# Kernel tuning notes

Measured on AMD Instinct MI355X. Metric: run time of the kernel, lower is better.

## Reference

```python
import jax, jax.numpy as jnp
import numpy as np

N_E = 8192
E_DIM = 64
BETA = 0.25
DIVERSITY_GAMMA = 1.0
INV_TEMP = 100.0
EPS = 1e-05


def _entropy(p):
    # matches torch: (-p * log(clamp(p, min=eps))).sum(-1)
    return (-p * jnp.log(jnp.clip(p, EPS))).sum(axis=-1)


def setup_inputs() -> dict:
    key = jax.random.key(0)
    k1, k2 = jax.random.split(key)
    z = jax.random.normal(k1, (16, E_DIM, 32, 32), dtype=jnp.float32)
    # codebook, init like nn.Embedding then uniform_(-1/n_e, 1/n_e) scale doesn't matter for math;
    # use a small uniform init faithful to the module
    emb = jax.random.uniform(k2, (N_E, E_DIM), dtype=jnp.float32,
                             minval=-1.0 / N_E, maxval=1.0 / N_E)
    return {"z": z, "emb": emb}


def reference(z, emb):
    sg = jax.lax.stop_gradient
    # b c h w -> b h w c
    zp = jnp.transpose(z, (0, 2, 3, 1))            # [B,H,W,C]
    zf = zp.reshape(-1, E_DIM)                      # [N, C]
    # pairwise squared distances: ||z||^2 + ||e||^2 - 2 z e^T
    d = (jnp.sum(zf * zf, axis=1, keepdims=True)
         + jnp.sum(emb * emb, axis=1)
         - 2.0 * jnp.einsum('nd,kd->nk', zf, emb))  # [N, n_e]
    min_indices = jnp.argmin(d, axis=1)             # [N]
    z_q = emb[min_indices].reshape(zp.shape)        # gather, [B,H,W,C]
    # legacy commitment loss
    loss = (jnp.mean((sg(z_q) - zp) ** 2)
            + BETA * jnp.mean((z_q - sg(zp)) ** 2))
    # entropy aux loss (frac_per_sample_entropy == 1.0)
    prob = jax.nn.softmax(-d * INV_TEMP, axis=-1)   # [N, n_e]
    per_sample_entropy = _entropy(prob).mean()
    avg_prob = prob.mean(axis=0)                    # [n_e]
    codebook_entropy = _entropy(avg_prob)
    entropy_aux = per_sample_entropy - DIVERSITY_GAMMA * codebook_entropy
    # straight-through estimator
    z_q = zp + sg(z_q - zp)
    quantized = jnp.transpose(z_q, (0, 3, 1, 2))    # b h w c -> b c h w
    return quantized, loss, entropy_aux, min_indices
```

## Files before the change

kernel.cpp:

```cpp
#include <hip/hip_runtime.h>
#include <cfloat>


typedef __attribute__((ext_vector_type(8))) short short8v;
typedef __attribute__((ext_vector_type(4))) float f32x4;

#define C100L2E 144.26950408889634f
#define C200L2E 288.53900817779268f
#define LN2 0.6931471805599453

#define BLOB_TILE 33792
#define OFF_BLOB   0
#define OFF_INVZ   2162688
#define OFF_MINIDX 2228224
#define OFF_AVG    2293760
#define OFF_PSE    2326528
#define OFF_ZPART  2326544
#define OFF_S1PART (OFF_ZPART + 262144)
#define OFF_DMPART (OFF_S1PART + 262144)
#define OFF_IMPART (OFF_DMPART + 262144)
#define OFF_LOSSP  (OFF_IMPART + 262144)
#define OFF_ZZ     (OFF_LOSSP + 32768)

__device__ __forceinline__ unsigned short f2bf_rne(float f) {
    unsigned u = __float_as_uint(f);
    u = (u + 0x7fffu + ((u >> 16) & 1u)) >> 16;
    return (unsigned short)u;
}

__device__ __forceinline__ void gload_lds16(const void* g, void* l) {
    __builtin_amdgcn_global_load_lds(
        (const __attribute__((address_space(1))) unsigned int*)g,
        (__attribute__((address_space(3))) unsigned int*)l, 16, 0, 0);
}

__global__ __launch_bounds__(256) void k_prep(const float* __restrict__ emb,
                                              char* __restrict__ blob) {
    const int k = blockIdx.x * 256 + threadIdx.x;
    const float* row = emb + k * 64;
    float fv[64];
#pragma unroll
    for (int i = 0; i < 16; ++i) {
        float4 v = ((const float4*)row)[i];
        fv[4 * i] = v.x; fv[4 * i + 1] = v.y; fv[4 * i + 2] = v.z; fv[4 * i + 3] = v.w;
    }
    float r8[8];
#pragma unroll
    for (int j = 0; j < 8; ++j) r8[j] = __fmul_rn(fv[j], fv[j]);
#pragma unroll
    for (int i = 8; i < 64; i += 8)
#pragma unroll
        for (int j = 0; j < 8; ++j)
            r8[j] = __fadd_rn(r8[j], __fmul_rn(fv[i + j], fv[i + j]));
    float s01 = __fadd_rn(r8[0], r8[1]), s23 = __fadd_rn(r8[2], r8[3]);
    float s45 = __fadd_rn(r8[4], r8[5]), s67 = __fadd_rn(r8[6], r8[7]);
    float e2 = __fadd_rn(__fadd_rn(s01, s23), __fadd_rn(s45, s67));

    char* tb = blob + (size_t)(k >> 7) * BLOB_TILE;
    const int r = k & 127;
    ((float*)(tb + 32768))[r] = e2;
    const int sw = (r & 7) << 4;
#pragma unroll
    for (int dh = 0; dh < 2; ++dh)
#pragma unroll
        for (int cg = 0; cg < 4; ++cg) {
            short8v hv, lv;
#pragma unroll
            for (int e = 0; e < 8; ++e) {
                float f = fv[dh * 32 + cg * 8 + e];
                unsigned short hb = f2bf_rne(f);
                float hf = __uint_as_float((unsigned)hb << 16);
                hv[e] = (short)hb;
                lv[e] = (short)f2bf_rne(f - hf);
            }
            const int byt = (r * 128 + dh * 64 + cg * 16) ^ sw;
            *(short8v*)(tb + byt) = hv;
            *(short8v*)(tb + 16384 + byt) = lv;
        }
}

__global__ __launch_bounds__(256) void k_zprep(const float* __restrict__ z,
                                               char* __restrict__ zblob,
                                               float* __restrict__ zz) {
    const int r = blockIdx.x * 256 + threadIdx.x;
    const float* src = z + (r >> 10) * 65536 + (r & 1023);
    float fv[64];
#pragma unroll
    for (int c = 0; c < 64; ++c) fv[c] = src[c * 1024];

    float r8[8];
#pragma unroll
    for (int j = 0; j < 8; ++j) r8[j] = __fmul_rn(fv[j], fv[j]);
#pragma unroll
    for (int i = 8; i < 64; i += 8)
#pragma unroll
        for (int j = 0; j < 8; ++j)
            r8[j] = __fadd_rn(r8[j], __fmul_rn(fv[i + j], fv[i + j]));
    float s01 = __fadd_rn(r8[0], r8[1]), s23 = __fadd_rn(r8[2], r8[3]);
    float s45 = __fadd_rn(r8[4], r8[5]), s67 = __fadd_rn(r8[6], r8[7]);
    zz[r] = __fadd_rn(__fadd_rn(s01, s23), __fadd_rn(s45, s67));

    char* tb = zblob + (size_t)(r >> 6) * 16384;
    const int rowp = r & 63;
#pragma unroll
    for (int cg = 0; cg < 8; ++cg) {
        short8v hv, lv;
#pragma unroll
        for (int e = 0; e < 8; ++e) {
            float f = fv[cg * 8 + e];
            unsigned short hb = f2bf_rne(f);
            float hf = __uint_as_float((unsigned)hb << 16);
            hv[e] = (short)hb;
            lv[e] = (short)f2bf_rne(f - hf);
        }
        *(short8v*)(tb + rowp * 128 + cg * 16) = hv;
        *(short8v*)(tb + 8192 + rowp * 128 + cg * 16) = lv;
    }
}

#define STAGE_EMB(DSTBASE, TILE)                                                  \
    {                                                                             \
        const char* gsrc = blob + (size_t)(TILE) * BLOB_TILE;                     \
        char* ldst = (DSTBASE) + ((tid >> 6) << 10);                              \
        const char* g = gsrc + tid * 16;                                          \
        _Pragma("unroll")                                                         \
        for (int q = 0; q < 8; ++q)                                               \
            gload_lds16(g + q * 4096, ldst + q * 4096);                           \
        if (tid < 32) gload_lds16(gsrc + 32768 + tid * 16, (DSTBASE) + 32768);    \
    }

#define STAGE512(DSTBASE, TILE)                                                   \
    {                                                                             \
        const char* gsrc = blob + (size_t)(TILE) * BLOB_TILE;                     \
        char* ldst = (DSTBASE) + ((tid >> 6) << 12);                              \
        const char* g = gsrc + ((tid >> 6) << 12) + (tid & 63) * 16;              \
        _Pragma("unroll")                                                         \
        for (int q = 0; q < 4; ++q)                                               \
            gload_lds16(g + q * 1024, ldst + q * 1024);                           \
        if (tid < 32) gload_lds16(gsrc + 32768 + tid * 16, (DSTBASE) + 32768);    \
    }

__global__ __launch_bounds__(512) void k_pass1(
    const char* __restrict__ zblob, const char* __restrict__ blob,
    const float* __restrict__ zz,
    float* __restrict__ Zpart, float* __restrict__ S1part,
    float* __restrict__ dmpart, int* __restrict__ impart)
{
    __shared__ __align__(16) char smem[2 * BLOB_TILE];

    const int tid = threadIdx.x;
    const int panel = blockIdx.x >> 2;
    const int ks = blockIdx.x & 3;
    const int n0 = panel * 128;

    const int ln = tid & 63, wv = tid >> 6;
    const int lr = ln & 15, lg = ln >> 4;

    short8v Ah[2], Al[2];
    {
        const int p64 = (n0 >> 6) + (wv >> 2);
        const int rowp = (wv & 3) * 16 + lr;
        const char* tb = zblob + (size_t)p64 * 16384;
#pragma unroll
        for (int s = 0; s < 2; ++s) {
            const int byt = rowp * 128 + s * 64 + lg * 16;
            Ah[s] = *(const short8v*)(tb + byt);
            Al[s] = *(const short8v*)(tb + 8192 + byt);
        }
    }
    float zzr[4];
#pragma unroll
    for (int rg = 0; rg < 4; ++rg)
        zzr[rg] = zz[n0 + wv * 16 + lg * 4 + rg];

    STAGE512(smem, ks * 16);

    float Zp[4] = {0.f, 0.f, 0.f, 0.f}, S1p[4] = {0.f, 0.f, 0.f, 0.f};
    float dmin[4] = {FLT_MAX, FLT_MAX, FLT_MAX, FLT_MAX};
    int imin[4] = {0, 0, 0, 0};

    for (int it = 0; it < 16; ++it) {
        const int kbase = ks * 2048 + it * 128;
        __syncthreads();
        const char* bb = smem + (it & 1) * BLOB_TILE;
        if (it < 15) STAGE512(smem + ((it + 1) & 1) * BLOB_TILE, ks * 16 + it + 1);

        f32x4 acc[8];
#pragma unroll
        for (int f = 0; f < 8; ++f) { f32x4 zv = {0.f, 0.f, 0.f, 0.f}; acc[f] = zv; }

#pragma unroll
        for (int f = 0; f < 8; ++f) {
            const int rr = f * 16 + lr;
            const int sw2 = (rr & 7) << 4;
            short8v Bh[2], Bl[2];
#pragma unroll
            for (int s = 0; s < 2; ++s) {
                const int byt = (rr * 128 + s * 64 + lg * 16) ^ sw2;
                Bh[s] = *(const short8v*)(bb + byt);
                Bl[s] = *(const short8v*)(bb + 16384 + byt);
            }
#pragma unroll
            for (int s = 0; s < 2; ++s) {
                acc[f] = __builtin_amdgcn_mfma_f32_16x16x32_bf16(Ah[s], Bh[s], acc[f], 0, 0, 0);
                acc[f] = __builtin_amdgcn_mfma_f32_16x16x32_bf16(Ah[s], Bl[s], acc[f], 0, 0, 0);
                acc[f] = __builtin_amdgcn_mfma_f32_16x16x32_bf16(Al[s], Bh[s], acc[f], 0, 0, 0);
                acc[f] = __builtin_amdgcn_mfma_f32_16x16x32_bf16(Al[s], Bl[s], acc[f], 0, 0, 0);
            }
        }

#pragma unroll
        for (int f = 0; f < 8; ++f) {
            const float e2v = *(const float*)(bb + 32768 + (f * 16 + lr) * 4);
            const float c2 = e2v * C100L2E;
            const int kk = kbase + f * 16 + lr;
#pragma unroll
            for (int rg = 0; rg < 4; ++rg) {
                const float sdot = acc[f][rg];
                const float t = fmaf(sdot, C200L2E, -c2);
                const float ex = __builtin_amdgcn_exp2f(t);
                Zp[rg] += ex;
                S1p[rg] = fmaf(t, ex, S1p[rg]);
                const float pre = __fadd_rn(zzr[rg], e2v);
                const float dnp = fmaf(-2.f, sdot, pre);
                if (dnp < dmin[rg]) { dmin[rg] = dnp; imin[rg] = kk; }
            }
        }
    }

#pragma unroll
    for (int msk = 1; msk < 16; msk <<= 1) {
#pragma unroll
        for (int rg = 0; rg < 4; ++rg) {
            float d2 = __shfl_xor(dmin[rg], msk, 16);
            int i2 = __shfl_xor(imin[rg], msk, 16);
            float Z2 = __shfl_xor(Zp[rg], msk, 16);
            float s2 = __shfl_xor(S1p[rg], msk, 16);
            if (d2 < dmin[rg] || (d2 == dmin[rg] && i2 < imin[rg])) {
                dmin[rg] = d2; imin[rg] = i2;
            }
            Zp[rg] += Z2;
            S1p[rg] += s2;
        }
    }
    if (lr == 0) {
#pragma unroll
        for (int rg = 0; rg < 4; ++rg) {
            const int n = n0 + wv * 16 + lg * 4 + rg;
            Zpart[ks * 16384 + n] = Zp[rg];
            S1part[ks * 16384 + n] = S1p[rg];
            dmpart[ks * 16384 + n] = dmin[rg];
            impart[ks * 16384 + n] = imin[rg];
        }
    }
}

__global__ __launch_bounds__(256) void k_rowred(
    const float* __restrict__ Zpart, const float* __restrict__ S1part,
    const float* __restrict__ dmpart, const int* __restrict__ impart,
    float* __restrict__ invZ, int* __restrict__ minidx,
    float* __restrict__ out_idx, double* __restrict__ pse_sum)
{
    const int n = blockIdx.x * 256 + threadIdx.x;
    float Z = __fadd_rn(__fadd_rn(Zpart[n], Zpart[16384 + n]),
                        __fadd_rn(Zpart[32768 + n], Zpart[49152 + n]));
    float S1 = __fadd_rn(__fadd_rn(S1part[n], S1part[16384 + n]),
                         __fadd_rn(S1part[32768 + n], S1part[49152 + n]));
    float dm = dmpart[n];
    int im = impart[n];
#pragma unroll
    for (int ksp = 1; ksp < 4; ++ksp) {
        float d2 = dmpart[ksp * 16384 + n];
        int i2 = impart[ksp * 16384 + n];
        if (d2 < dm || (d2 == dm && i2 < im)) { dm = d2; im = i2; }
    }
    minidx[n] = im;
    out_idx[n] = (float)im;
    float iz = 1.0f / Z;
    invZ[n] = iz;
    double h = log((double)Z) - LN2 * (double)S1 * (double)iz;
#pragma unroll
    for (int m = 32; m > 0; m >>= 1) h += __shfl_xor(h, m, 64);
    if ((threadIdx.x & 63) == 0) atomicAdd(pse_sum, h);
}

__global__ __launch_bounds__(256) void k_pass2(
    const char* __restrict__ zblob, const char* __restrict__ blob,
    const float* __restrict__ invZ, float* __restrict__ avg_acc)
{
    __shared__ __align__(16) char smem[BLOB_TILE + 4096];
    float* izAll = (float*)(smem + BLOB_TILE);

    const int tid = threadIdx.x;
    const int kt = blockIdx.x & 63;
    const int ns = blockIdx.x >> 6;
    const int ln = tid & 63, wv = tid >> 6;
    const int lr = ln & 15, lg = ln >> 4;

    STAGE_EMB(smem, kt);
    gload_lds16((const char*)(invZ + ns * 1024) + tid * 16,
                (char*)izAll + (wv << 10));
    __syncthreads();

    float e2v[8];
#pragma unroll
    for (int f = 0; f < 8; ++f)
        e2v[f] = *(const float*)(smem + 32768 + (f * 16 + lr) * 4);

    float acck[8] = {0.f, 0.f, 0.f, 0.f, 0.f, 0.f, 0.f, 0.f};

    for (int it = 0; it < 8; ++it) {
        short8v Ah[2][2], Al[2][2];
        const int p64 = ns * 16 + it * 2 + (wv >> 1);
        const char* tb = zblob + (size_t)p64 * 16384;
#pragma unroll
        for (int m = 0; m < 2; ++m) {
            const int rowp = (wv & 1) * 32 + m * 16 + lr;
#pragma unroll
            for (int s = 0; s < 2; ++s) {
                const int byt = rowp * 128 + s * 64 + lg * 16;
                Ah[m][s] = *(const short8v*)(tb + byt);
                Al[m][s] = *(const short8v*)(tb + 8192 + byt);
            }
        }
        const int izb = it * 128 + wv * 32 + lg * 4;
        float4 iz0 = *(const float4*)&izAll[izb];
        float4 iz1 = *(const float4*)&izAll[izb + 16];
        float izr[2][4] = {{iz0.x, iz0.y, iz0.z, iz0.w},
                           {iz1.x, iz1.y, iz1.z, iz1.w}};

        f32x4 acc[2][8];
#pragma unroll
        for (int m = 0; m < 2; ++m)
#pragma unroll
            for (int f = 0; f < 8; ++f) {
                f32x4 zv = {0.f, 0.f, 0.f, 0.f};
                acc[m][f] = zv;
            }

#pragma unroll
        for (int f = 0; f < 8; ++f) {
            const int rr = f * 16 + lr;
            const int sw2 = (rr & 7) << 4;
            short8v Bh[2], Bl[2];
#pragma unroll
            for (int s = 0; s < 2; ++s) {
                const int byt = (rr * 128 + s * 64 + lg * 16) ^ sw2;
                Bh[s] = *(const short8v*)(smem + byt);
                Bl[s] = *(const short8v*)(smem + 16384 + byt);
            }
#pragma unroll
            for (int s = 0; s < 2; ++s)
#pragma unroll
                for (int m = 0; m < 2; ++m) {
                    acc[m][f] = __builtin_amdgcn_mfma_f32_16x16x32_bf16(Ah[m][s], Bh[s], acc[m][f], 0, 0, 0);
                    acc[m][f] = __builtin_amdgcn_mfma_f32_16x16x32_bf16(Ah[m][s], Bl[s], acc[m][f], 0, 0, 0);
                    acc[m][f] = __builtin_amdgcn_mfma_f32_16x16x32_bf16(Al[m][s], Bh[s], acc[m][f], 0, 0, 0);
                    acc[m][f] = __builtin_amdgcn_mfma_f32_16x16x32_bf16(Al[m][s], Bl[s], acc[m][f], 0, 0, 0);
                }
        }

#pragma unroll
        for (int f = 0; f < 8; ++f) {
            const float c2 = e2v[f] * C100L2E;
#pragma unroll
            for (int m = 0; m < 2; ++m)
#pragma unroll
                for (int rg = 0; rg < 4; ++rg) {
                    const float t = fmaf(acc[m][f][rg], C200L2E, -c2);
                    const float ex = __builtin_amdgcn_exp2f(t);
                    acck[f] = fmaf(ex, izr[m][rg], acck[f]);
                }
        }
    }

#pragma unroll
    for (int f = 0; f < 8; ++f) {
        float cs = acck[f];
        cs += __shfl_xor(cs, 16, 64);
        cs += __shfl_xor(cs, 32, 64);
        if (lg == 0) atomicAdd(&avg_acc[kt * 128 + f * 16 + lr], cs);
    }
}

__global__ __launch_bounds__(256) void k_quant(
    const float* __restrict__ z, const float* __restrict__ emb,
    const int* __restrict__ minidx, float* __restrict__ out,
    double* __restrict__ loss_part)
{
    __shared__ float lred[4];
    const int o = blockIdx.x * 256 + threadIdx.x;
    const int n = ((o >> 16) << 10) + (o & 1023);
    const int c = (o >> 10) & 63;
    const int idx = minidx[n];
    const float e = emb[idx * 64 + c];
    const float zv = z[o];
    out[o] = e;
    float d = e - zv;
    float sq = d * d;
#pragma unroll
    for (int m = 32; m > 0; m >>= 1) sq += __shfl_xor(sq, m, 64);
    if ((threadIdx.x & 63) == 0) lred[threadIdx.x >> 6] = sq;
    __syncthreads();
    if (threadIdx.x == 0)
        loss_part[blockIdx.x] = (double)lred[0] + (double)lred[1]
                              + (double)lred[2] + (double)lred[3];
}

__global__ __launch_bounds__(256) void k_final(
    const float* __restrict__ avg_acc, const double* __restrict__ pse_sum,
    const double* __restrict__ loss_part, float* __restrict__ out)
{
    __shared__ double red[256];
    const int tid = threadIdx.x;

    double lsum = 0.0;
    for (int k = tid; k < 4096; k += 256) lsum += loss_part[k];
    red[tid] = lsum;
    __syncthreads();
    for (int s = 128; s > 0; s >>= 1) {
        if (tid < s) red[tid] += red[tid + s];
        __syncthreads();
    }
    double ltot = red[0];
    __syncthreads();

    double local = 0.0;
    for (int k = tid; k < 8192; k += 256) {
        float p = avg_acc[k] * (1.0f / 16384.0f);
        float cl = fmaxf(p, 1e-5f);
        local += (double)(-p * logf(cl));
    }
    red[tid] = local;
    __syncthreads();
    for (int s = 128; s > 0; s >>= 1) {
        if (tid < s) red[tid] += red[tid + s];
        __syncthreads();
    }
    if (tid == 0) {
        double ce = red[0];
        double pse = pse_sum[0] / 16384.0;
        out[1048576] = (float)(1.25 * ltot / 1048576.0);
        out[1048577] = (float)(pse - ce);
    }
}

extern "C" void kernel_launch(void* const* d_in, const int* in_sizes, int n_in,
                              void* d_out, int out_size, void* d_ws, size_t ws_size,
                              hipStream_t stream) {
    const float* z = (const float*)d_in[0];
    const float* emb = (const float*)d_in[1];
    float* out = (float*)d_out;
    char* ws = (char*)d_ws;
    char* blob = ws + OFF_BLOB;
    float* invZ = (float*)(ws + OFF_INVZ);
    int* minidx = (int*)(ws + OFF_MINIDX);
    float* avg_acc = (float*)(ws + OFF_AVG);
    double* pse_sum = (double*)(ws + OFF_PSE);
    float* Zpart = (float*)(ws + OFF_ZPART);
    float* S1part = (float*)(ws + OFF_S1PART);
    float* dmpart = (float*)(ws + OFF_DMPART);
    int* impart = (int*)(ws + OFF_IMPART);
    double* loss_part = (double*)(ws + OFF_LOSSP);
    float* zz = (float*)(ws + OFF_ZZ);
    char* zblob = (char*)d_out;

    hipMemsetAsync(ws + OFF_AVG, 0, 32768 + 16, stream);

    k_prep<<<32, 256, 0, stream>>>(emb, blob);
    k_zprep<<<64, 256, 0, stream>>>(z, zblob, zz);
    k_pass1<<<512, 512, 0, stream>>>(zblob, blob, zz, Zpart, S1part, dmpart, impart);
    k_rowred<<<64, 256, 0, stream>>>(Zpart, S1part, dmpart, impart,
                                     invZ, minidx, out + 1048578, pse_sum);
    k_pass2<<<1024, 256, 0, stream>>>(zblob, blob, invZ, avg_acc);
    k_quant<<<4096, 256, 0, stream>>>(z, emb, minidx, out, loss_part);
    k_final<<<1, 256, 0, stream>>>(avg_acc, pse_sum, loss_part, out);
}
```

Before: 187.3 us.

## Merge prep kernels, double pass1 row tile per wave, precompute scaled codebook norms

Combines the codebook and z preprocessing kernels into a single launch to remove one kernel launch. In pass1 each wave now handles 32 rows instead of 16, so every codebook tile staged in LDS and every B fragment is reused across two MFMA row blocks, and the grid is halved to 256 blocks. The codebook norm is also stored pre-multiplied by 100/ln2 in the blob and staged into LDS, which saves a multiply per element in both passes. The costs are higher register pressure in pass1 and fewer blocks, which could reduce occupancy and latency hiding.

```diff
diff --git a/kernel.cpp b/kernel.cpp
--- a/kernel.cpp
+++ b/kernel.cpp
@@ -34,87 +34,88 @@
         (__attribute__((address_space(3))) unsigned int*)l, 16, 0, 0);
 }
 
-__global__ __launch_bounds__(256) void k_prep(const float* __restrict__ emb,
-                                              char* __restrict__ blob) {
-    const int k = blockIdx.x * 256 + threadIdx.x;
-    const float* row = emb + k * 64;
-    float fv[64];
-#pragma unroll
-    for (int i = 0; i < 16; ++i) {
-        float4 v = ((const float4*)row)[i];
-        fv[4 * i] = v.x; fv[4 * i + 1] = v.y; fv[4 * i + 2] = v.z; fv[4 * i + 3] = v.w;
-    }
-    float r8[8];
-#pragma unroll
-    for (int j = 0; j < 8; ++j) r8[j] = __fmul_rn(fv[j], fv[j]);
-#pragma unroll
-    for (int i = 8; i < 64; i += 8)
-#pragma unroll
-        for (int j = 0; j < 8; ++j)
-            r8[j] = __fadd_rn(r8[j], __fmul_rn(fv[i + j], fv[i + j]));
-    float s01 = __fadd_rn(r8[0], r8[1]), s23 = __fadd_rn(r8[2], r8[3]);
-    float s45 = __fadd_rn(r8[4], r8[5]), s67 = __fadd_rn(r8[6], r8[7]);
-    float e2 = __fadd_rn(__fadd_rn(s01, s23), __fadd_rn(s45, s67));
-
-    char* tb = blob + (size_t)(k >> 7) * BLOB_TILE;
-    const int r = k & 127;
-    ((float*)(tb + 32768))[r] = e2;
-    const int sw = (r & 7) << 4;
-#pragma unroll
-    for (int dh = 0; dh < 2; ++dh)
-#pragma unroll
-        for (int cg = 0; cg < 4; ++cg) {
+__global__ __launch_bounds__(256) void k_prep(
+    const float* __restrict__ emb, const float* __restrict__ z,
+    char* __restrict__ blob, char* __restrict__ zblob, float* __restrict__ zz)
+{
+    if (blockIdx.x < 32) {
+        const int k = blockIdx.x * 256 + threadIdx.x;
+        const float* row = emb + k * 64;
+        float fv[64];
+#pragma unroll
+        for (int i = 0; i < 16; ++i) {
+            float4 v = ((const float4*)row)[i];
+            fv[4 * i] = v.x; fv[4 * i + 1] = v.y; fv[4 * i + 2] = v.z; fv[4 * i + 3] = v.w;
+        }
+        float r8[8];
+#pragma unroll
+        for (int j = 0; j < 8; ++j) r8[j] = __fmul_rn(fv[j], fv[j]);
+#pragma unroll
+        for (int i = 8; i < 64; i += 8)
+#pragma unroll
+            for (int j = 0; j < 8; ++j)
+                r8[j] = __fadd_rn(r8[j], __fmul_rn(fv[i + j], fv[i + j]));
+        float s01 = __fadd_rn(r8[0], r8[1]), s23 = __fadd_rn(r8[2], r8[3]);
+        float s45 = __fadd_rn(r8[4], r8[5]), s67 = __fadd_rn(r8[6], r8[7]);
+        float e2 = __fadd_rn(__fadd_rn(s01, s23), __fadd_rn(s45, s67));
+
+        char* tb = blob + (size_t)(k >> 7) * BLOB_TILE;
+        const int r = k & 127;
+        ((float*)(tb + 32768))[r] = e2;
+        ((float*)(tb + 33280))[r] = e2 * C100L2E;
+        const int sw = (r & 7) << 4;
+#pragma unroll
+        for (int dh = 0; dh < 2; ++dh)
+#pragma unroll
+            for (int cg = 0; cg < 4; ++cg) {
+                short8v hv, lv;
+#pragma unroll
+                for (int e = 0; e < 8; ++e) {
+                    float f = fv[dh * 32 + cg * 8 + e];
+                    unsigned short hb = f2bf_rne(f);
+                    float hf = __uint_as_float((unsigned)hb << 16);
+                    hv[e] = (short)hb;
+                    lv[e] = (short)f2bf_rne(f - hf);
+                }
+                const int byt = (r * 128 + dh * 64 + cg * 16) ^ sw;
+                *(short8v*)(tb + byt) = hv;
+                *(short8v*)(tb + 16384 + byt) = lv;
+            }
+    } else {
+        const int r = (blockIdx.x - 32) * 256 + threadIdx.x;
+        const float* src = z + (r >> 10) * 65536 + (r & 1023);
+        float fv[64];
+#pragma unroll
+        for (int c = 0; c < 64; ++c) fv[c] = src[c * 1024];
+
+        float r8[8];
+#pragma unroll
+        for (int j = 0; j < 8; ++j) r8[j] = __fmul_rn(fv[j], fv[j]);
+#pragma unroll
+        for (int i = 8; i < 64; i += 8)
+#pragma unroll
+            for (int j = 0; j < 8; ++j)
+                r8[j] = __fadd_rn(r8[j], __fmul_rn(fv[i + j], fv[i + j]));
+        float s01 = __fadd_rn(r8[0], r8[1]), s23 = __fadd_rn(r8[2], r8[3]);
+        float s45 = __fadd_rn(r8[4], r8[5]), s67 = __fadd_rn(r8[6], r8[7]);
+        zz[r] = __fadd_rn(__fadd_rn(s01, s23), __fadd_rn(s45, s67));
+
+        char* tb = zblob + (size_t)(r >> 6) * 16384;
+        const int rowp = r & 63;
+#pragma unroll
+        for (int cg = 0; cg < 8; ++cg) {
             short8v hv, lv;
 #pragma unroll
             for (int e = 0; e < 8; ++e) {
-                float f = fv[dh * 32 + cg * 8 + e];
+                float f = fv[cg * 8 + e];
                 unsigned short hb = f2bf_rne(f);
                 float hf = __uint_as_float((unsigned)hb << 16);
                 hv[e] = (short)hb;
                 lv[e] = (short)f2bf_rne(f - hf);
             }
-            const int byt = (r * 128 + dh * 64 + cg * 16) ^ sw;
-            *(short8v*)(tb + byt) = hv;
-            *(short8v*)(tb + 16384 + byt) = lv;
-        }
-}
-
-__global__ __launch_bounds__(256) void k_zprep(const float* __restrict__ z,
-                                               char* __restrict__ zblob,
-                                               float* __restrict__ zz) {
-    const int r = blockIdx.x * 256 + threadIdx.x;
-    const float* src = z + (r >> 10) * 65536 + (r & 1023);
-    float fv[64];
-#pragma unroll
-    for (int c = 0; c < 64; ++c) fv[c] = src[c * 1024];
-
-    float r8[8];
-#pragma unroll
-    for (int j = 0; j < 8; ++j) r8[j] = __fmul_rn(fv[j], fv[j]);
-#pragma unroll
-    for (int i = 8; i < 64; i += 8)
-#pragma unroll
-        for (int j = 0; j < 8; ++j)
-            r8[j] = __fadd_rn(r8[j], __fmul_rn(fv[i + j], fv[i + j]));
-    float s01 = __fadd_rn(r8[0], r8[1]), s23 = __fadd_rn(r8[2], r8[3]);
-    float s45 = __fadd_rn(r8[4], r8[5]), s67 = __fadd_rn(r8[6], r8[7]);
-    zz[r] = __fadd_rn(__fadd_rn(s01, s23), __fadd_rn(s45, s67));
-
-    char* tb = zblob + (size_t)(r >> 6) * 16384;
-    const int rowp = r & 63;
-#pragma unroll
-    for (int cg = 0; cg < 8; ++cg) {
-        short8v hv, lv;
-#pragma unroll
-        for (int e = 0; e < 8; ++e) {
-            float f = fv[cg * 8 + e];
-            unsigned short hb = f2bf_rne(f);
-            float hf = __uint_as_float((unsigned)hb << 16);
-            hv[e] = (short)hb;
-            lv[e] = (short)f2bf_rne(f - hf);
-        }
-        *(short8v*)(tb + rowp * 128 + cg * 16) = hv;
-        *(short8v*)(tb + 8192 + rowp * 128 + cg * 16) = lv;
+            *(short8v*)(tb + rowp * 128 + cg * 16) = hv;
+            *(short8v*)(tb + 8192 + rowp * 128 + cg * 16) = lv;
+        }
     }
 }
 
@@ -126,7 +127,8 @@
         _Pragma("unroll")                                                         \
         for (int q = 0; q < 8; ++q)                                               \
             gload_lds16(g + q * 4096, ldst + q * 4096);                           \
-        if (tid < 32) gload_lds16(gsrc + 32768 + tid * 16, (DSTBASE) + 32768);    \
+        if (tid < 64) gload_lds16(gsrc + 32768 + (tid & 63) * 16,                 \
+                                  (DSTBASE) + 32768);                             \
     }
 
 #define STAGE512(DSTBASE, TILE)                                                   \
@@ -137,7 +139,8 @@
         _Pragma("unroll")                                                         \
         for (int q = 0; q < 4; ++q)                                               \
             gload_lds16(g + q * 1024, ldst + q * 1024);                           \
-        if (tid < 32) gload_lds16(gsrc + 32768 + tid * 16, (DSTBASE) + 32768);    \
+        if (tid < 64) gload_lds16(gsrc + 32768 + (tid & 63) * 16,                 \
+                                  (DSTBASE) + 32768);                             \
     }
 
 __global__ __launch_bounds__(512) void k_pass1(
@@ -151,33 +154,44 @@
     const int tid = threadIdx.x;
     const int panel = blockIdx.x >> 2;
     const int ks = blockIdx.x & 3;
-    const int n0 = panel * 128;
+    const int n0 = panel * 256;
 
     const int ln = tid & 63, wv = tid >> 6;
     const int lr = ln & 15, lg = ln >> 4;
 
-    short8v Ah[2], Al[2];
+    short8v Ah[2][2], Al[2][2];
     {
-        const int p64 = (n0 >> 6) + (wv >> 2);
-        const int rowp = (wv & 3) * 16 + lr;
+        const int p64 = (n0 >> 6) + (wv >> 1);
         const char* tb = zblob + (size_t)p64 * 16384;
 #pragma unroll
-        for (int s = 0; s < 2; ++s) {
-            const int byt = rowp * 128 + s * 64 + lg * 16;
-            Ah[s] = *(const short8v*)(tb + byt);
-            Al[s] = *(const short8v*)(tb + 8192 + byt);
-        }
-    }
-    float zzr[4];
-#pragma unroll
-    for (int rg = 0; rg < 4; ++rg)
-        zzr[rg] = zz[n0 + wv * 16 + lg * 4 + rg];
+        for (int m = 0; m < 2; ++m) {
+            const int rowp = (wv & 1) * 32 + m * 16 + lr;
+#pragma unroll
+            for (int s = 0; s < 2; ++s) {
+                const int byt = rowp * 128 + s * 64 + lg * 16;
+                Ah[m][s] = *(const short8v*)(tb + byt);
+                Al[m][s] = *(const short8v*)(tb + 8192 + byt);
+            }
+        }
+    }
+    float zzr[2][4];
+#pragma unroll
+    for (int m = 0; m < 2; ++m)
+#pragma unroll
+        for (int rg = 0; rg < 4; ++rg)
+            zzr[m][rg] = zz[n0 + wv * 32 + m * 16 + lg * 4 + rg];
 
     STAGE512(smem, ks * 16);
 
-    float Zp[4] = {0.f, 0.f, 0.f, 0.f}, S1p[4] = {0.f, 0.f, 0.f, 0.f};
-    float dmin[4] = {FLT_MAX, FLT_MAX, FLT_MAX, FLT_MAX};
-    int imin[4] = {0, 0, 0, 0};
+    float Zp[2][4], S1p[2][4], dmin[2][4];
+    int imin[2][4];
+#pragma unroll
+    for (int m = 0; m < 2; ++m)
+#pragma unroll
+        for (int rg = 0; rg < 4; ++rg) {
+            Zp[m][rg] = 0.f; S1p[m][rg] = 0.f;
+            dmin[m][rg] = FLT_MAX; imin[m][rg] = 0;
+        }
 
     for (int it = 0; it < 16; ++it) {
         const int kbase = ks * 2048 + it * 128;
@@ -185,10 +199,6 @@
         const char* bb = smem + (it & 1) * BLOB_TILE;
         if (it < 15) STAGE512(smem + ((it + 1) & 1) * BLOB_TILE, ks * 16 + it + 1);
 
-        f32x4 acc[8];
-#pragma unroll
-        for (int f = 0; f < 8; ++f) { f32x4 zv = {0.f, 0.f, 0.f, 0.f}; acc[f] = zv; }
-
 #pragma unroll
         for (int f = 0; f < 8; ++f) {
             const int rr = f * 16 + lr;
@@ -200,58 +210,67 @@
                 Bh[s] = *(const short8v*)(bb + byt);
                 Bl[s] = *(const short8v*)(bb + 16384 + byt);
             }
+            f32x4 a0 = {0.f, 0.f, 0.f, 0.f}, a1 = {0.f, 0.f, 0.f, 0.f};
 #pragma unroll
             for (int s = 0; s < 2; ++s) {
-                acc[f] = __builtin_amdgcn_mfma_f32_16x16x32_bf16(Ah[s], Bh[s], acc[f], 0, 0, 0);
-                acc[f] = __builtin_amdgcn_mfma_f32_16x16x32_bf16(Ah[s], Bl[s], acc[f], 0, 0, 0);
-                acc[f] = __builtin_amdgcn_mfma_f32_16x16x32_bf16(Al[s], Bh[s], acc[f], 0, 0, 0);
-                acc[f] = __builtin_amdgcn_mfma_f32_16x16x32_bf16(Al[s], Bl[s], acc[f], 0, 0, 0);
-            }
-        }
-
-#pragma unroll
-        for (int f = 0; f < 8; ++f) {
+                a0 = __builtin_amdgcn_mfma_f32_16x16x32_bf16(Ah[0][s], Bh[s], a0, 0, 0, 0);
+                a0 = __builtin_amdgcn_mfma_f32_16x16x32_bf16(Ah[0][s], Bl[s], a0, 0, 0, 0);
+                a0 = __builtin_amdgcn_mfma_f32_16x16x32_bf16(Al[0][s], Bh[s], a0, 0, 0, 0);
+                a0 = __builtin_amdgcn_mfma_f32_16x16x32_bf16(Al[0][s], Bl[s], a0, 0, 0, 0);
+                a1 = __builtin_amdgcn_mfma_f32_16x16x32_bf16(Ah[1][s], Bh[s], a1, 0, 0, 0);
+                a1 = __builtin_amdgcn_mfma_f32_16x16x32_bf16(Ah[1][s], Bl[s], a1, 0, 0, 0);
+                a1 = __builtin_amdgcn_mfma_f32_16x16x32_bf16(Al[1][s], Bh[s], a1, 0, 0, 0);
+                a1 = __builtin_amdgcn_mfma_f32_16x16x32_bf16(Al[1][s], Bl[s], a1, 0, 0, 0);
+            }
+
             const float e2v = *(const float*)(bb + 32768 + (f * 16 + lr) * 4);
-            const float c2 = e2v * C100L2E;
+            const float c2 = *(const float*)(bb + 33280 + (f * 16 + lr) * 4);
             const int kk = kbase + f * 16 + lr;
 #pragma unroll
+            for (int m = 0; m < 2; ++m) {
+#pragma unroll
+                for (int rg = 0; rg < 4; ++rg) {
+                    const float sdot = (m == 0) ? a0[rg] : a1[rg];
+                    const float t = fmaf(sdot, C200L2E, -c2);
+                    const float ex = __builtin_amdgcn_exp2f(t);
+                    Zp[m][rg] += ex;
+                    S1p[m][rg] = fmaf(t, ex, S1p[m][rg]);
+                    const float pre = __fadd_rn(zzr[m][rg], e2v);
+                    const float dnp = fmaf(-2.f, sdot, pre);
+                    if (dnp < dmin[m][rg]) { dmin[m][rg] = dnp; imin[m][rg] = kk; }
+                }
+            }
+        }
+    }
+
+#pragma unroll
+    for (int msk = 1; msk < 16; msk <<= 1) {
+#pragma unroll
+        for (int m = 0; m < 2; ++m)
+#pragma unroll
             for (int rg = 0; rg < 4; ++rg) {
-                const float sdot = acc[f][rg];
-                const float t = fmaf(sdot, C200L2E, -c2);
-                const float ex = __builtin_amdgcn_exp2f(t);
-                Zp[rg] += ex;
-                S1p[rg] = fmaf(t, ex, S1p[rg]);
-                const float pre = __fadd_rn(zzr[rg], e2v);
-                const float dnp = fmaf(-2.f, sdot, pre);
-                if (dnp < dmin[rg]) { dmin[rg] = dnp; imin[rg] = kk; }
-            }
-        }
-    }
-
-#pragma unroll
-    for (int msk = 1; msk < 16; msk <<= 1) {
-#pragma unroll
-        for (int rg = 0; rg < 4; ++rg) {
-            float d2 = __shfl_xor(dmin[rg], msk, 16);
-            int i2 = __shfl_xor(imin[rg], msk, 16);
-            float Z2 = __shfl_xor(Zp[rg], msk, 16);
-            float s2 = __shfl_xor(S1p[rg], msk, 16);
-            if (d2 < dmin[rg] || (d2 == dmin[rg] && i2 < imin[rg])) {
-                dmin[rg] = d2; imin[rg] = i2;
-            }
-            Zp[rg] += Z2;
-            S1p[rg] += s2;
-        }
+                float d2 = __shfl_xor(dmin[m][rg], msk, 16);
+                int i2 = __shfl_xor(imin[m][rg], msk, 16);
+                float Z2 = __shfl_xor(Zp[m][rg], msk, 16);
+                float s2 = __shfl_xor(S1p[m][rg], msk, 16);
+                if (d2 < dmin[m][rg] || (d2 == dmin[m][rg] && i2 < imin[m][rg])) {
+                    dmin[m][rg] = d2; imin[m][rg] = i2;
+                }
+                Zp[m][rg] += Z2;
+                S1p[m][rg] += s2;
+            }
     }
     if (lr == 0) {
 #pragma unroll
-        for (int rg = 0; rg < 4; ++rg) {
-            const int n = n0 + wv * 16 + lg * 4 + rg;
-            Zpart[ks * 16384 + n] = Zp[rg];
-            S1part[ks * 16384 + n] = S1p[rg];
-            dmpart[ks * 16384 + n] = dmin[rg];
-            impart[ks * 16384 + n] = imin[rg];
-        }
+        for (int m = 0; m < 2; ++m)
+#pragma unroll
+            for (int rg = 0; rg < 4; ++rg) {
+                const int n = n0 + wv * 32 + m * 16 + lg * 4 + rg;
+                Zpart[ks * 16384 + n] = Zp[m][rg];
+                S1part[ks * 16384 + n] = S1p[m][rg];
+                dmpart[ks * 16384 + n] = dmin[m][rg];
+                impart[ks * 16384 + n] = imin[m][rg];
+            }
     }
 }
 
@@ -302,10 +321,10 @@
                 (char*)izAll + (wv << 10));
     __syncthreads();
 
-    float e2v[8];
+    float c2v[8];
 #pragma unroll
     for (int f = 0; f < 8; ++f)
-        e2v[f] = *(const float*)(smem + 32768 + (f * 16 + lr) * 4);
+        c2v[f] = *(const float*)(smem + 33280 + (f * 16 + lr) * 4);
 
     float acck[8] = {0.f, 0.f, 0.f, 0.f, 0.f, 0.f, 0.f, 0.f};
 
@@ -362,12 +381,11 @@
 
 #pragma unroll
         for (int f = 0; f < 8; ++f) {
-            const float c2 = e2v[f] * C100L2E;
 #pragma unroll
             for (int m = 0; m < 2; ++m)
 #pragma unroll
                 for (int rg = 0; rg < 4; ++rg) {
-                    const float t = fmaf(acc[m][f][rg], C200L2E, -c2);
+                    const float t = fmaf(acc[m][f][rg], C200L2E, -c2v[f]);
                     const float ex = __builtin_amdgcn_exp2f(t);
                     acck[f] = fmaf(ex, izr[m][rg], acck[f]);
                 }
@@ -467,9 +485,8 @@
 
     hipMemsetAsync(ws + OFF_AVG, 0, 32768 + 16, stream);
 
-    k_prep<<<32, 256, 0, stream>>>(emb, blob);
-    k_zprep<<<64, 256, 0, stream>>>(z, zblob, zz);
-    k_pass1<<<512, 512, 0, stream>>>(zblob, blob, zz, Zpart, S1part, dmpart, impart);
+    k_prep<<<96, 256, 0, stream>>>(emb, z, blob, zblob, zz);
+    k_pass1<<<256, 512, 0, stream>>>(zblob, blob, zz, Zpart, S1part, dmpart, impart);
     k_rowred<<<64, 256, 0, stream>>>(Zpart, S1part, dmpart, impart,
                                      invZ, minidx, out + 1048578, pse_sum);
     k_pass2<<<1024, 256, 0, stream>>>(zblob, blob, invZ, avg_acc);
```

New measurement: 178.2 us. 1.05x faster.
